# Performance work log

Hardware: AMD Instinct MI355X
Metric: run time of the kernel (lower is better)

The kernel has to match this reference:

```python
import jax, jax.numpy as jnp
from jax import lax
import numpy as np

# Module config (from init_kwargs / torch defaults)
CONF_THRES = 0.25
IOU_THRES = 0.45
MAX_DET = 300          # torch non_max_suppression max_det
BATCH = 16
N_PRED = 25200         # YOLOv5 anchors @ 640x640
NC = 80                # COCO classes
IMG = 640.0


def setup_inputs() -> dict:
    key = jax.random.key(0)
    k1, k2 = jax.random.split(key)
    # raw YOLO head output: [xywh (pixels), obj in [0,1], 80 class probs in [0,1]]
    prediction = jax.random.uniform(k1, (BATCH, N_PRED, NC + 5), dtype=jnp.float32)
    prediction = prediction.at[:, :, :4].multiply(IMG)  # realistic pixel-scale boxes
    logits = jax.random.normal(k2, (BATCH, N_PRED, NC), dtype=jnp.float32)
    return {"prediction": prediction, "logits": logits}


def _xywh2xyxy(x):
    xy, wh = x[..., :2], x[..., 2:4]
    return jnp.concatenate([xy - wh * 0.5, xy + wh * 0.5], axis=-1)


def _nms_image(pred, logit):
    """pred: [N, 85], logit: [N, 80] -> [MAX_DET, 87] padded detections.

    Row layout: [x1, y1, x2, y2, conf, cls, objectness, logits(80)].
    Invalid (padding) rows are zeroed, matching the variable-length torch output.
    """
    obj = pred[:, 4]                              # [N]
    cls_conf = pred[:, 5:] * obj[:, None]         # conf = cls_prob * obj  [N, 80]
    conf = jnp.max(cls_conf, axis=1)              # best-class confidence
    cls = jnp.argmax(cls_conf, axis=1)
    boxes = _xywh2xyxy(pred[:, :4])               # [N, 4] xyxy
    # candidate mask: obj > conf_thres (xc) AND best conf > conf_thres (conf_mask)
    valid = (obj > CONF_THRES) & (conf > CONF_THRES)
    scores0 = jnp.where(valid, conf, -jnp.inf)
    area = (boxes[:, 2] - boxes[:, 0]) * (boxes[:, 3] - boxes[:, 1])  # [N]

    # agnostic NMS (agnostic_nms=True -> no per-class box offset)
    def step(sc, _):
        idx = jnp.argmax(sc)                      # highest remaining score
        ok = jnp.isfinite(sc[idx])                # any candidate left?
        b = boxes[idx]
        lt = jnp.maximum(b[:2], boxes[:, :2])
        rb = jnp.minimum(b[2:], boxes[:, 2:])
        wh = jnp.clip(rb - lt, 0.0)
        inter = wh[:, 0] * wh[:, 1]
        iou = inter / (area[idx] + area - inter + 1e-9)
        sc = jnp.where(iou > IOU_THRES, -jnp.inf, sc)  # suppress (incl. self)
        return sc, (idx, ok)

    _, (sel, ok) = lax.scan(step, scores0, None, length=MAX_DET)

    det = jnp.concatenate(
        [boxes[sel], conf[sel][:, None], cls[sel][:, None].astype(jnp.float32),
         obj[sel][:, None], logit[sel]], axis=1)  # [MAX_DET, 87]
    return det * ok[:, None].astype(det.dtype)


def reference(prediction, logits):
    # [B, MAX_DET, 87]: xyxy(4) | conf | cls | objectness | class logits(80)
    return jax.vmap(_nms_image)(prediction, logits)
```

## Files before the change

kernel.cpp:

```cpp
#include <hip/hip_runtime.h>
#include <math.h>

#define NPRED  25200
#define BATCH  16
#define NC     80
#define MAXDET 300
#define NDIM   87
#define NBIN   1024

#define WS_SC      0
#define WS_BOX     1612800
#define WS_SELIDX  8064000
#define WS_SELCNT  8083200
#define WS_HIST    8083264
#define WS_CURSOR  8148800
#define WS_IA      8214336
#define WS_BINNED  8279872

#define PREP_TPB 256
#define PB 128

__global__ __launch_bounds__(PREP_TPB)
void prep_kernel(const float* __restrict__ pred,
                 float* __restrict__ sc,
                 float4* __restrict__ box,
                 unsigned int* __restrict__ hist) {
    __shared__ float4 s4[PB * 85 / 4];
    float* s = (float*)s4;
    const int t = threadIdx.x;
    const float4* p4 = (const float4*)(pred + (size_t)blockIdx.x * (PB * 85));
    for (int i = t; i < PB * 85 / 4; i += PREP_TPB) s4[i] = p4[i];
    __syncthreads();
    if (t < PB) {
        const float* row = s + t * 85;
        float x = row[0], y = row[1], w = row[2], h = row[3], obj = row[4];
        float best = -INFINITY;
        #pragma unroll 8
        for (int c = 0; c < NC; ++c) {
            float v = __fmul_rn(row[5 + c], obj);
            if (v > best) best = v;
        }
        float hw = __fmul_rn(w, 0.5f), hh = __fmul_rn(h, 0.5f);
        bool valid = (obj > 0.25f) && (best > 0.25f);
        int g = blockIdx.x * PB + t;
        sc[g]  = valid ? best : -INFINITY;
        box[g] = make_float4(__fsub_rn(x, hw), __fsub_rn(y, hh),
                             __fadd_rn(x, hw), __fadd_rn(y, hh));
        if (valid) {
            int img = g / NPRED;
            unsigned int sb = __float_as_uint(best);
            int bin = min((int)((sb - 0x3E800000u) >> 14), NBIN - 1);
            atomicAdd(&hist[img * NBIN + bin], 1u);
        }
    }
}

__global__ __launch_bounds__(NBIN)
void scan_kernel(const unsigned int* __restrict__ hist,
                 unsigned int* __restrict__ IaG,
                 unsigned int* __restrict__ cursor) {
    __shared__ unsigned int sA[NBIN], sB[NBIN];
    const int img = blockIdx.x, t = threadIdx.x;
    unsigned int cnt = hist[img * NBIN + t];
    sA[t] = cnt;
    __syncthreads();
    unsigned int *src = sA, *dst = sB;
    for (int d = 1; d < NBIN; d <<= 1) {
        dst[t] = src[t] + ((t + d) < NBIN ? src[t + d] : 0u);
        __syncthreads();
        unsigned int* tmp = src; src = dst; dst = tmp;
    }
    IaG[img * NBIN + t]    = src[t];
    cursor[img * NBIN + t] = src[t] - cnt;
}

#define SCB  16
#define STPB 512

__global__ __launch_bounds__(STPB)
void scatter_kernel(const float* __restrict__ sc,
                    unsigned int* __restrict__ cursor,
                    unsigned long long* __restrict__ binned) {
    const int img = blockIdx.x / SCB, part = blockIdx.x % SCB;
    const float* sci = sc + (size_t)img * NPRED;
    for (int e = part * STPB + threadIdx.x; e < NPRED; e += SCB * STPB) {
        float s = sci[e];
        if (s != -INFINITY) {
            unsigned int sb = __float_as_uint(s);
            int bin = min((int)((sb - 0x3E800000u) >> 14), NBIN - 1);
            unsigned int pos = atomicAdd(&cursor[img * NBIN + bin], 1u);
            binned[(size_t)img * NPRED + pos] =
                ((unsigned long long)(~sb) << 32) | (unsigned int)e;
        }
    }
}

#define TPB      1024
#define TCAP     4096
#define FIRSTCAP 1024
#define SLOTS    4
#define NW       (TPB / 64)

__device__ __forceinline__ bool iou_gt(float Bx1, float By1, float Bx2, float By2,
                                       float BA,
                                       float cx1, float cy1, float cx2, float cy2,
                                       float ca, double K) {
    float lx = fmaxf(Bx1, cx1), ly = fmaxf(By1, cy1);
    float rx = fminf(Bx2, cx2), ry = fminf(By2, cy2);
    float ww = fmaxf(__fsub_rn(rx, lx), 0.0f);
    float hh = fmaxf(__fsub_rn(ry, ly), 0.0f);
    float inter = __fmul_rn(ww, hh);
    float denom = __fadd_rn(__fsub_rn(__fadd_rn(BA, ca), inter), 1e-9f);
    return ((double)inter > K * (double)denom);
}

__device__ __forceinline__ int blk_min(int v, int* s_red, int t, int wid) {
    #pragma unroll
    for (int off = 32; off; off >>= 1) v = min(v, __shfl_down(v, off));
    if ((t & 63) == 0) s_red[wid] = v;
    __syncthreads();
    int r = s_red[0];
    #pragma unroll
    for (int w = 1; w < NW; ++w) r = min(r, s_red[w]);
    return r;
}

__global__ __launch_bounds__(TPB)
void nms_kernel(const unsigned long long* __restrict__ binned,
                const unsigned int* __restrict__ IaG,
                const float4* __restrict__ box_g,
                int* __restrict__ selidx,
                int* __restrict__ selcnt) {
    __shared__ unsigned long long sbuf[TCAP];
    __shared__ unsigned int IaL[NBIN];
    __shared__ float4 kbox[MAXDET];
    __shared__ float  karea[MAXDET];
    __shared__ unsigned char s_alive[TCAP];
    __shared__ int s_red[NW];
    __shared__ int s_kept, s_sticky, s_stickyIdx, s_fillFrom, s_cnt2;

    const int img = blockIdx.x, t = threadIdx.x, wid = t >> 6;
    const float4* bxi = box_g + (size_t)img * NPRED;
    const unsigned long long* bin_img = binned + (size_t)img * NPRED;
    const double K = (double)0.45f + 0x1p-26;

    IaL[t] = IaG[img * NBIN + t];
    if (t == 0) { s_kept = 0; s_sticky = 0; }
    __syncthreads();
    const int n_valid = (int)IaL[0];

    int o = 0, b_hi = NBIN;
    bool firstT = true;
    for (;;) {
        if (s_kept >= MAXDET || s_sticky || o >= n_valid) break;

        const int cap = firstT ? FIRSTCAP : TCAP;
        __syncthreads();
        int vb = (t < b_hi && ((int)IaL[t] - o) <= cap) ? t : 0x7FFFFFFF;
        int b_lo = blk_min(vb, s_red, t, wid);
        if (b_lo == 0x7FFFFFFF && cap != TCAP) {
            __syncthreads();
            vb = (t < b_hi && ((int)IaL[t] - o) <= TCAP) ? t : 0x7FFFFFFF;
            b_lo = blk_min(vb, s_red, t, wid);
        }
        int c;
        if (b_lo != 0x7FFFFFFF) {
            c = (int)IaL[b_lo] - o;
        } else {
            __syncthreads();
            vb = (t < b_hi && ((int)IaL[t] - o) > 0) ? -t : 0x7FFFFFFF;
            int m2 = blk_min(vb, s_red, t, wid);
            b_lo = -m2;
            c = min((int)IaL[b_lo] - o, TCAP);
        }
        if (c <= 0) break;

        unsigned int um = 0;
        unsigned long long ukey[SLOTS];
        #pragma unroll
        for (int s = 0; s < SLOTS; ++s) {
            int p = s * TPB + t;
            bool av = (p < c);
            ukey[s] = av ? bin_img[o + p] : ~0ULL;
            if (av) um |= (1u << s);
        }
        const int kept0 = s_kept;

        if (kept0 > 0 && um) {
            float ux1[SLOTS], uy1[SLOTS], ux2[SLOTS], uy2[SLOTS], uar[SLOTS];
            #pragma unroll
            for (int s = 0; s < SLOTS; ++s) {
                unsigned int ix = (um & (1u << s)) ? (unsigned int)ukey[s] : 0u;
                float4 b = bxi[ix];
                ux1[s] = b.x; uy1[s] = b.y; ux2[s] = b.z; uy2[s] = b.w;
                uar[s] = __fmul_rn(__fsub_rn(b.z, b.x), __fsub_rn(b.w, b.y));
            }
            for (int kb = 0; kb < kept0; ++kb) {
                float4 B = kbox[kb];
                float BA = karea[kb];
                #pragma unroll
                for (int s = 0; s < SLOTS; ++s) {
                    if (um & (1u << s)) {
                        if (iou_gt(B.x, B.y, B.z, B.w, BA,
                                   ux1[s], uy1[s], ux2[s], uy2[s], uar[s], K))
                            um &= ~(1u << s);
                    }
                }
                if (!um) break;
            }
        }
        if (t == 0) s_cnt2 = 0;
        __syncthreads();
        int cnt2;
        if (kept0 == 0) {
            #pragma unroll
            for (int s = 0; s < SLOTS; ++s) {
                int p = s * TPB + t;
                if (p < c) sbuf[p] = ukey[s];
            }
            cnt2 = c;
            __syncthreads();
        } else {
            #pragma unroll
            for (int s = 0; s < SLOTS; ++s)
                if (um & (1u << s)) sbuf[atomicAdd(&s_cnt2, 1)] = ukey[s];
            __syncthreads();
            cnt2 = s_cnt2;
        }

        if (cnt2 > 0) {
            int m = 1; while (m < cnt2) m <<= 1;
            for (int p = t; p < m; p += TPB) if (p >= cnt2) sbuf[p] = ~0ULL;
            __syncthreads();
            for (int k = 2; k <= m; k <<= 1) {
                for (int j = k >> 1; j > 0; j >>= 1) {
                    for (int i = t; i < m; i += TPB) {
                        int l = i ^ j;
                        if (l > i) {
                            unsigned long long a = sbuf[i], b2 = sbuf[l];
                            if ((a > b2) == ((i & k) == 0)) { sbuf[i] = b2; sbuf[l] = a; }
                        }
                    }
                    __syncthreads();
                }
            }
            unsigned int rm = 0;
            float rx1[SLOTS], ry1[SLOTS], rx2[SLOTS], ry2[SLOTS], rar[SLOTS];
            #pragma unroll
            for (int s = 0; s < SLOTS; ++s) {
                int p = t * SLOTS + s;
                bool av = (p < cnt2);
                unsigned int ix = av ? (unsigned int)sbuf[p] : 0u;
                float4 b = bxi[ix];
                rx1[s] = b.x; ry1[s] = b.y; rx2[s] = b.z; ry2[s] = b.w;
                rar[s] = __fmul_rn(__fsub_rn(b.z, b.x), __fsub_rn(b.w, b.y));
                if (av) rm |= (1u << s);
                s_alive[p] = av ? 1 : 0;
            }
            __syncthreads();

            const int nwin = (cnt2 + 63) >> 6;
            int applied = kept0;
            for (int g = 0; g < nwin; ++g) {
                int k0 = s_kept;
                if (rm) {
                    for (int kb = applied; kb < k0; ++kb) {
                        float4 B = kbox[kb];
                        float BA = karea[kb];
                        #pragma unroll
                        for (int s = 0; s < SLOTS; ++s) {
                            if (rm & (1u << s)) {
                                if (iou_gt(B.x, B.y, B.z, B.w, BA,
                                           rx1[s], ry1[s], rx2[s], ry2[s], rar[s], K)) {
                                    rm &= ~(1u << s);
                                    s_alive[t * SLOTS + s] = 0;
                                }
                            }
                        }
                        if (!rm) break;
                    }
                }
                applied = k0;
                __syncthreads();
                if (t < 64) {
                    int p = g * 64 + t;
                    int a = s_alive[p];
                    unsigned int ix = a ? (unsigned int)sbuf[p] : 0u;
                    float4 b = bxi[ix];
                    float cx1 = b.x, cy1 = b.y, cx2 = b.z, cy2 = b.w;
                    float car = __fmul_rn(__fsub_rn(b.z, b.x), __fsub_rn(b.w, b.y));
                    int kept = k0;
                    for (;;) {
                        unsigned long long bal = __ballot(a != 0);
                        if (!bal) break;
                        int f = (int)__builtin_ctzll(bal);
                        float Bx1 = __shfl(cx1, f), By1 = __shfl(cy1, f);
                        float Bx2 = __shfl(cx2, f), By2 = __shfl(cy2, f);
                        float BA  = __shfl(car, f);
                        int bidx  = __shfl((int)ix, f);
                        if (t == f) a = 0;
                        if (t == 0) {
                            selidx[img * MAXDET + kept] = bidx;
                            kbox[kept] = make_float4(Bx1, By1, Bx2, By2);
                            karea[kept] = BA;
                        }
                        float dns = __fadd_rn(__fsub_rn(__fadd_rn(BA, BA), BA), 1e-9f);
                        if (!((double)BA > K * (double)dns)) {
                            if (t == 0) { s_sticky = 1; s_stickyIdx = bidx; s_fillFrom = kept + 1; }
                            kept = MAXDET;
                            break;
                        }
                        if (a) {
                            if (iou_gt(Bx1, By1, Bx2, By2, BA,
                                       cx1, cy1, cx2, cy2, car, K)) a = 0;
                        }
                        ++kept;
                        if (kept >= MAXDET) break;
                    }
                    if (t == 0) s_kept = kept;
                }
                __syncthreads();
                if (((t * SLOTS) >> 6) == g) rm = 0;
                if (s_kept >= MAXDET || s_sticky) break;
            }
        }
        o = (int)IaL[b_lo];
        b_hi = b_lo;
        firstT = false;
    }
    int keptF = s_kept;
    if (s_sticky) {
        for (int k2 = s_fillFrom + t; k2 < MAXDET; k2 += TPB)
            selidx[img * MAXDET + k2] = s_stickyIdx;
        keptF = MAXDET;
    }
    if (t == 0) selcnt[img] = keptF;
}

#define GT 256

__global__ __launch_bounds__(GT)
void gather_kernel(const float* __restrict__ pred,
                   const float4* __restrict__ box,
                   const float* __restrict__ logits,
                   const int* __restrict__ selidx,
                   const int* __restrict__ selcnt,
                   float* __restrict__ out) {
    int tid = blockIdx.x * GT + threadIdx.x;
    if (tid >= BATCH * MAXDET * NDIM) return;
    int row = tid / NDIM, col = tid - row * NDIM;
    int img = row / MAXDET, det = row - img * MAXDET;
    float v = 0.0f;
    if (det < selcnt[img]) {
        int s = selidx[img * MAXDET + det];
        size_t g = (size_t)img * NPRED + s;
        if (col < 4) {
            float4 b = box[g];
            v = (col == 0) ? b.x : (col == 1) ? b.y : (col == 2) ? b.z : b.w;
        } else if (col == 6) {
            v = pred[g * 85 + 4];
        } else if (col >= 7) {
            v = logits[g * NC + (col - 7)];
        } else {
            const float* p = pred + g * 85;
            float obj = p[4];
            float best = -INFINITY; int bc = 0;
            #pragma unroll 8
            for (int c = 0; c < NC; ++c) {
                float q = __fmul_rn(p[5 + c], obj);
                if (q > best) { best = q; bc = c; }
            }
            v = (col == 4) ? best : (float)bc;
        }
    }
    out[tid] = v;
}

extern "C" void kernel_launch(void* const* d_in, const int* in_sizes, int n_in,
                              void* d_out, int out_size, void* d_ws, size_t ws_size,
                              hipStream_t stream) {
    const float* pred   = (const float*)d_in[0];
    const float* logits = (const float*)d_in[1];
    float* out = (float*)d_out;

    char* ws = (char*)d_ws;
    float*              sc     = (float*)(ws + WS_SC);
    float4*             box    = (float4*)(ws + WS_BOX);
    int*                selidx = (int*)(ws + WS_SELIDX);
    int*                selcnt = (int*)(ws + WS_SELCNT);
    unsigned int*       hist   = (unsigned int*)(ws + WS_HIST);
    unsigned int*       cursor = (unsigned int*)(ws + WS_CURSOR);
    unsigned int*       IaG    = (unsigned int*)(ws + WS_IA);
    unsigned long long* binned = (unsigned long long*)(ws + WS_BINNED);

    hipMemsetAsync(hist, 0, BATCH * NBIN * sizeof(unsigned int), stream);

    prep_kernel<<<BATCH * NPRED / PB, PREP_TPB, 0, stream>>>(pred, sc, box, hist);
    scan_kernel<<<BATCH, NBIN, 0, stream>>>(hist, IaG, cursor);
    scatter_kernel<<<BATCH * SCB, STPB, 0, stream>>>(sc, cursor, binned);
    nms_kernel<<<BATCH, TPB, 0, stream>>>(binned, IaG, box, selidx, selcnt);
    int gtot = BATCH * MAXDET * NDIM;
    gather_kernel<<<(gtot + GT - 1) / GT, GT, 0, stream>>>(pred, box, logits, selidx, selcnt, out);
}
```

Before: 303.8 us.

## Pre-sort histogram bins in a parallel kernel and drop in-loop bitonic sort

Adds a binsort kernel that sorts each score bin in place across many blocks, so the single-block-per-image NMS loop no longer runs a shared-memory bitonic sort on every tile. The NMS kernel now uses a contiguous per-wave slot layout with up to 8 slots per thread, ballot-based stream compaction instead of atomics, and greedy selection run inside a window wave that holds its boxes in registers. It also raises the tile capacity to 8192. The cost is one extra kernel launch over 16K blocks, more register pressure from 8 slots of box data, and partial-bin tile handling.

New measurement: 655.9 us. 2.16x slower.

```diff
diff --git a/kernel.cpp b/kernel.cpp
--- a/kernel.cpp
+++ b/kernel.cpp
@@ -95,10 +95,61 @@
     }
 }
 
+#define BS_TPB 256
+#define BS_CAP 4096
+
+__global__ __launch_bounds__(BS_TPB)
+void binsort_kernel(const unsigned int* __restrict__ hist,
+                    const unsigned int* __restrict__ IaG,
+                    unsigned long long* __restrict__ binned) {
+    __shared__ unsigned long long lds[BS_CAP];
+    const int img = blockIdx.x >> 10, b = blockIdx.x & (NBIN - 1);
+    const int t = threadIdx.x;
+    const int cnt = (int)hist[img * NBIN + b];
+    if (cnt <= 1) return;
+    const int start = (int)IaG[img * NBIN + b] - cnt;
+    unsigned long long* ptr = binned + (size_t)img * NPRED + start;
+
+    if (cnt <= 64) {
+        if (t < 64) {
+            unsigned long long key = (t < cnt) ? ptr[t] : ~0ULL;
+            #pragma unroll
+            for (int k = 2; k <= 64; k <<= 1) {
+                #pragma unroll
+                for (int j = k >> 1; j > 0; j >>= 1) {
+                    unsigned long long other = __shfl_xor(key, j);
+                    bool up = ((t & k) == 0), lower = ((t & j) == 0);
+                    unsigned long long mn = min(key, other), mx = max(key, other);
+                    key = (up == lower) ? mn : mx;
+                }
+            }
+            if (t < cnt) ptr[t] = key;
+        }
+        return;
+    }
+    const int cap = min(cnt, BS_CAP);
+    int m = 64; while (m < cap) m <<= 1;
+    for (int i = t; i < m; i += BS_TPB) lds[i] = (i < cap) ? ptr[i] : ~0ULL;
+    __syncthreads();
+    for (int k = 2; k <= m; k <<= 1) {
+        for (int j = k >> 1; j > 0; j >>= 1) {
+            for (int i = t; i < m; i += BS_TPB) {
+                int l = i ^ j;
+                if (l > i) {
+                    unsigned long long a = lds[i], b2 = lds[l];
+                    if ((a > b2) == ((i & k) == 0)) { lds[i] = b2; lds[l] = a; }
+                }
+            }
+            __syncthreads();
+        }
+    }
+    for (int i = t; i < cap; i += BS_TPB) ptr[i] = lds[i];
+}
+
 #define TPB      1024
-#define TCAP     4096
+#define TCAP     8192
 #define FIRSTCAP 1024
-#define SLOTS    4
+#define MAXS     8
 #define NW       (TPB / 64)
 
 __device__ __forceinline__ bool iou_gt(float Bx1, float By1, float Bx2, float By2,
@@ -115,6 +166,7 @@
 }
 
 __device__ __forceinline__ int blk_min(int v, int* s_red, int t, int wid) {
+    __syncthreads();
     #pragma unroll
     for (int off = 32; off; off >>= 1) v = min(v, __shfl_down(v, off));
     if ((t & 63) == 0) s_red[wid] = v;
@@ -135,14 +187,17 @@
     __shared__ unsigned int IaL[NBIN];
     __shared__ float4 kbox[MAXDET];
     __shared__ float  karea[MAXDET];
-    __shared__ unsigned char s_alive[TCAP];
     __shared__ int s_red[NW];
-    __shared__ int s_kept, s_sticky, s_stickyIdx, s_fillFrom, s_cnt2;
-
-    const int img = blockIdx.x, t = threadIdx.x, wid = t >> 6;
+    __shared__ unsigned int s_wsum[NW];
+    __shared__ int s_kept, s_sticky, s_stickyIdx, s_fillFrom;
+
+    const int img = blockIdx.x, t = threadIdx.x, wid = t >> 6, lane = t & 63;
     const float4* bxi = box_g + (size_t)img * NPRED;
     const unsigned long long* bin_img = binned + (size_t)img * NPRED;
     const double K = (double)0.45f + 0x1p-26;
+    const unsigned long long lmask = (lane == 63) ? ~0ULL >> 1 : (1ULL << (lane + 1)) - 1;
+    const unsigned long long below = lmask >> 1 << 1 >> 1;
+    (void)below;
 
     IaL[t] = IaG[img * NBIN + t];
     if (t == 0) { s_kept = 0; s_sticky = 0; }
@@ -152,14 +207,13 @@
     int o = 0, b_hi = NBIN;
     bool firstT = true;
     for (;;) {
+        __syncthreads();
         if (s_kept >= MAXDET || s_sticky || o >= n_valid) break;
 
         const int cap = firstT ? FIRSTCAP : TCAP;
-        __syncthreads();
         int vb = (t < b_hi && ((int)IaL[t] - o) <= cap) ? t : 0x7FFFFFFF;
         int b_lo = blk_min(vb, s_red, t, wid);
         if (b_lo == 0x7FFFFFFF && cap != TCAP) {
-            __syncthreads();
             vb = (t < b_hi && ((int)IaL[t] - o) <= TCAP) ? t : 0x7FFFFFFF;
             b_lo = blk_min(vb, s_red, t, wid);
         }
@@ -167,7 +221,6 @@
         if (b_lo != 0x7FFFFFFF) {
             c = (int)IaL[b_lo] - o;
         } else {
-            __syncthreads();
             vb = (t < b_hi && ((int)IaL[t] - o) > 0) ? -t : 0x7FFFFFFF;
             int m2 = blk_min(vb, s_red, t, wid);
             b_lo = -m2;
@@ -175,31 +228,30 @@
         }
         if (c <= 0) break;
 
+        const int S = (c + 1023) >> 10;
         unsigned int um = 0;
-        unsigned long long ukey[SLOTS];
+        unsigned long long ukey[MAXS];
+        float ux1[MAXS], uy1[MAXS], ux2[MAXS], uy2[MAXS], uar[MAXS];
         #pragma unroll
-        for (int s = 0; s < SLOTS; ++s) {
-            int p = s * TPB + t;
-            bool av = (p < c);
-            ukey[s] = av ? bin_img[o + p] : ~0ULL;
+        for (int s = 0; s < MAXS; ++s) {
+            int p = wid * (S << 6) + (s << 6) + lane;
+            bool av = (s < S) && (p < c);
+            unsigned long long key = av ? bin_img[o + p] : ~0ULL;
+            ukey[s] = key;
+            unsigned int ix = av ? (unsigned int)key : 0u;
+            float4 b = bxi[ix];
+            ux1[s] = b.x; uy1[s] = b.y; ux2[s] = b.z; uy2[s] = b.w;
+            uar[s] = __fmul_rn(__fsub_rn(b.z, b.x), __fsub_rn(b.w, b.y));
             if (av) um |= (1u << s);
         }
         const int kept0 = s_kept;
 
         if (kept0 > 0 && um) {
-            float ux1[SLOTS], uy1[SLOTS], ux2[SLOTS], uy2[SLOTS], uar[SLOTS];
-            #pragma unroll
-            for (int s = 0; s < SLOTS; ++s) {
-                unsigned int ix = (um & (1u << s)) ? (unsigned int)ukey[s] : 0u;
-                float4 b = bxi[ix];
-                ux1[s] = b.x; uy1[s] = b.y; ux2[s] = b.z; uy2[s] = b.w;
-                uar[s] = __fmul_rn(__fsub_rn(b.z, b.x), __fsub_rn(b.w, b.y));
-            }
             for (int kb = 0; kb < kept0; ++kb) {
                 float4 B = kbox[kb];
                 float BA = karea[kb];
                 #pragma unroll
-                for (int s = 0; s < SLOTS; ++s) {
+                for (int s = 0; s < MAXS; ++s) {
                     if (um & (1u << s)) {
                         if (iou_gt(B.x, B.y, B.z, B.w, BA,
                                    ux1[s], uy1[s], ux2[s], uy2[s], uar[s], K))
@@ -209,123 +261,124 @@
                 if (!um) break;
             }
         }
-        if (t == 0) s_cnt2 = 0;
+
+        int myoff[MAXS];
+        unsigned int wcnt = 0;
+        #pragma unroll
+        for (int s = 0; s < MAXS; ++s) {
+            unsigned long long bal = __ballot((int)((um >> s) & 1u));
+            unsigned long long lt = (lane == 0) ? 0ULL : (~0ULL >> (64 - lane));
+            myoff[s] = (int)(wcnt + __popcll(bal & lt));
+            wcnt += (unsigned int)__popcll(bal);
+        }
+        if (lane == 0) s_wsum[wid] = wcnt;
         __syncthreads();
-        int cnt2;
-        if (kept0 == 0) {
+        int wbase = 0, cnt2 = 0;
+        #pragma unroll
+        for (int w = 0; w < NW; ++w) {
+            int v = (int)s_wsum[w];
+            if (w < wid) wbase += v;
+            cnt2 += v;
+        }
+        #pragma unroll
+        for (int s = 0; s < MAXS; ++s)
+            if (um & (1u << s)) sbuf[wbase + myoff[s]] = ukey[s];
+        __syncthreads();
+
+        if (cnt2 > 0) {
+            const int S2 = (cnt2 >= 512) ? 8 : max(1, (cnt2 + 63) >> 6);
+            const int W = S2 << 6;
+            const int nwin = (cnt2 + W - 1) / W;
+            unsigned int rm = 0;
+            unsigned int rIdx[MAXS];
+            float rx1[MAXS], ry1[MAXS], rx2[MAXS], ry2[MAXS], rar[MAXS];
             #pragma unroll
-            for (int s = 0; s < SLOTS; ++s) {
-                int p = s * TPB + t;
-                if (p < c) sbuf[p] = ukey[s];
-            }
-            cnt2 = c;
-            __syncthreads();
-        } else {
-            #pragma unroll
-            for (int s = 0; s < SLOTS; ++s)
-                if (um & (1u << s)) sbuf[atomicAdd(&s_cnt2, 1)] = ukey[s];
-            __syncthreads();
-            cnt2 = s_cnt2;
-        }
-
-        if (cnt2 > 0) {
-            int m = 1; while (m < cnt2) m <<= 1;
-            for (int p = t; p < m; p += TPB) if (p >= cnt2) sbuf[p] = ~0ULL;
-            __syncthreads();
-            for (int k = 2; k <= m; k <<= 1) {
-                for (int j = k >> 1; j > 0; j >>= 1) {
-                    for (int i = t; i < m; i += TPB) {
-                        int l = i ^ j;
-                        if (l > i) {
-                            unsigned long long a = sbuf[i], b2 = sbuf[l];
-                            if ((a > b2) == ((i & k) == 0)) { sbuf[i] = b2; sbuf[l] = a; }
-                        }
-                    }
-                    __syncthreads();
-                }
-            }
-            unsigned int rm = 0;
-            float rx1[SLOTS], ry1[SLOTS], rx2[SLOTS], ry2[SLOTS], rar[SLOTS];
-            #pragma unroll
-            for (int s = 0; s < SLOTS; ++s) {
-                int p = t * SLOTS + s;
-                bool av = (p < cnt2);
-                unsigned int ix = av ? (unsigned int)sbuf[p] : 0u;
+            for (int s = 0; s < MAXS; ++s) {
+                int p = wid * W + (s << 6) + lane;
+                bool av = (s < S2) && (p < cnt2);
+                unsigned long long key = av ? sbuf[p] : ~0ULL;
+                unsigned int ix = av ? (unsigned int)key : 0u;
+                rIdx[s] = ix;
                 float4 b = bxi[ix];
                 rx1[s] = b.x; ry1[s] = b.y; rx2[s] = b.z; ry2[s] = b.w;
                 rar[s] = __fmul_rn(__fsub_rn(b.z, b.x), __fsub_rn(b.w, b.y));
                 if (av) rm |= (1u << s);
-                s_alive[p] = av ? 1 : 0;
-            }
-            __syncthreads();
-
-            const int nwin = (cnt2 + 63) >> 6;
-            int applied = kept0;
+            }
+
             for (int g = 0; g < nwin; ++g) {
-                int k0 = s_kept;
+                const int k0 = s_kept;
+                if (wid == g) {
+                    int kept = k0;
+                    for (;;) {
+                        int bestp = 0x7FFFFFFF;
+                        #pragma unroll
+                        for (int s = 0; s < MAXS; ++s) {
+                            if (s < S2) {
+                                unsigned long long bal = __ballot((int)((rm >> s) & 1u));
+                                if (bal) bestp = min(bestp, (s << 6) | (int)__builtin_ctzll(bal));
+                            }
+                        }
+                        if (bestp == 0x7FFFFFFF) break;
+                        const int fs = bestp >> 6, f = bestp & 63;
+                        float Bx1 = 0, By1 = 0, Bx2 = 0, By2 = 0, BA = 0; int bidx = 0;
+                        #pragma unroll
+                        for (int s = 0; s < MAXS; ++s) if (s == fs) {
+                            Bx1 = __shfl(rx1[s], f); By1 = __shfl(ry1[s], f);
+                            Bx2 = __shfl(rx2[s], f); By2 = __shfl(ry2[s], f);
+                            BA  = __shfl(rar[s], f); bidx = __shfl((int)rIdx[s], f);
+                        }
+                        if (lane == f) rm &= ~(1u << fs);
+                        if (lane == 0) {
+                            selidx[img * MAXDET + kept] = bidx;
+                            kbox[kept] = make_float4(Bx1, By1, Bx2, By2);
+                            karea[kept] = BA;
+                        }
+                        float dns = __fadd_rn(__fsub_rn(__fadd_rn(BA, BA), BA), 1e-9f);
+                        if (!((double)BA > K * (double)dns)) {
+                            if (lane == 0) { s_sticky = 1; s_stickyIdx = bidx; s_fillFrom = kept + 1; }
+                            kept = MAXDET;
+                            break;
+                        }
+                        #pragma unroll
+                        for (int s = 0; s < MAXS; ++s) {
+                            if (s < S2) {
+                                if (__ballot((int)((rm >> s) & 1u))) {
+                                    if ((rm >> s) & 1u) {
+                                        if (iou_gt(Bx1, By1, Bx2, By2, BA,
+                                                   rx1[s], ry1[s], rx2[s], ry2[s], rar[s], K))
+                                            rm &= ~(1u << s);
+                                    }
+                                }
+                            }
+                        }
+                        ++kept;
+                        if (kept >= MAXDET) break;
+                    }
+                    if (lane == 0) s_kept = kept;
+                }
+                __syncthreads();
+                if (s_sticky || s_kept >= MAXDET) break;
+                const int k1 = s_kept;
                 if (rm) {
-                    for (int kb = applied; kb < k0; ++kb) {
+                    for (int kb = k0; kb < k1; ++kb) {
                         float4 B = kbox[kb];
                         float BA = karea[kb];
                         #pragma unroll
-                        for (int s = 0; s < SLOTS; ++s) {
+                        for (int s = 0; s < MAXS; ++s) {
                             if (rm & (1u << s)) {
                                 if (iou_gt(B.x, B.y, B.z, B.w, BA,
-                                           rx1[s], ry1[s], rx2[s], ry2[s], rar[s], K)) {
+                                           rx1[s], ry1[s], rx2[s], ry2[s], rar[s], K))
                                     rm &= ~(1u << s);
-                                    s_alive[t * SLOTS + s] = 0;
-                                }
                             }
                         }
                         if (!rm) break;
                     }
                 }
-                applied = k0;
                 __syncthreads();
-                if (t < 64) {
-                    int p = g * 64 + t;
-                    int a = s_alive[p];
-                    unsigned int ix = a ? (unsigned int)sbuf[p] : 0u;
-                    float4 b = bxi[ix];
-                    float cx1 = b.x, cy1 = b.y, cx2 = b.z, cy2 = b.w;
-                    float car = __fmul_rn(__fsub_rn(b.z, b.x), __fsub_rn(b.w, b.y));
-                    int kept = k0;
-                    for (;;) {
-                        unsigned long long bal = __ballot(a != 0);
-                        if (!bal) break;
-                        int f = (int)__builtin_ctzll(bal);
-                        float Bx1 = __shfl(cx1, f), By1 = __shfl(cy1, f);
-                        float Bx2 = __shfl(cx2, f), By2 = __shfl(cy2, f);
-                        float BA  = __shfl(car, f);
-                        int bidx  = __shfl((int)ix, f);
-                        if (t == f) a = 0;
-                        if (t == 0) {
-                            selidx[img * MAXDET + kept] = bidx;
-                            kbox[kept] = make_float4(Bx1, By1, Bx2, By2);
-                            karea[kept] = BA;
-                        }
-                        float dns = __fadd_rn(__fsub_rn(__fadd_rn(BA, BA), BA), 1e-9f);
-                        if (!((double)BA > K * (double)dns)) {
-                            if (t == 0) { s_sticky = 1; s_stickyIdx = bidx; s_fillFrom = kept + 1; }
-                            kept = MAXDET;
-                            break;
-                        }
-                        if (a) {
-                            if (iou_gt(Bx1, By1, Bx2, By2, BA,
-                                       cx1, cy1, cx2, cy2, car, K)) a = 0;
-                        }
-                        ++kept;
-                        if (kept >= MAXDET) break;
-                    }
-                    if (t == 0) s_kept = kept;
-                }
-                __syncthreads();
-                if (((t * SLOTS) >> 6) == g) rm = 0;
-                if (s_kept >= MAXDET || s_sticky) break;
-            }
-        }
-        o = (int)IaL[b_lo];
-        b_hi = b_lo;
+            }
+        }
+        o += c;
+        if (o >= (int)IaL[b_lo]) b_hi = b_lo;
         firstT = false;
     }
     int keptF = s_kept;
@@ -398,6 +451,7 @@
     prep_kernel<<<BATCH * NPRED / PB, PREP_TPB, 0, stream>>>(pred, sc, box, hist);
     scan_kernel<<<BATCH, NBIN, 0, stream>>>(hist, IaG, cursor);
     scatter_kernel<<<BATCH * SCB, STPB, 0, stream>>>(sc, cursor, binned);
+    binsort_kernel<<<BATCH * NBIN, BS_TPB, 0, stream>>>(hist, IaG, binned);
     nms_kernel<<<BATCH, TPB, 0, stream>>>(binned, IaG, box, selidx, selcnt);
     int gtot = BATCH * MAXDET * NDIM;
     gather_kernel<<<(gtot + GT - 1) / GT, GT, 0, stream>>>(pred, box, logits, selidx, selcnt, out);
```

## Pre-sort score bins in parallel kernel and drop in-block bitonic sort from NMS

Applied to the files above, without the earlier changes.

Adds a binsort kernel that sorts each histogram bin of candidates in parallel across many blocks, using wave shuffles for small bins and LDS bitonic sort for larger ones. The NMS kernel can then skip its serial per-tile bitonic sort, since the keys already arrive in order. The atomic compaction of survivors is replaced by an order-preserving ballot/popcount prefix compaction, and the tile loads are reorganised per wave. The cost is an extra launch of 16K blocks, most of which exit immediately. Bins larger than 4096 entries are only partially sorted, which may be a correctness risk for degenerate inputs.

Measured after the change: 321.6 us. 5.8% more time.

```diff
diff --git a/kernel.cpp b/kernel.cpp
--- a/kernel.cpp
+++ b/kernel.cpp
@@ -95,6 +95,57 @@
     }
 }
 
+#define BS_TPB 256
+#define BS_CAP 4096
+
+__global__ __launch_bounds__(BS_TPB)
+void binsort_kernel(const unsigned int* __restrict__ hist,
+                    const unsigned int* __restrict__ IaG,
+                    unsigned long long* __restrict__ binned) {
+    __shared__ unsigned long long lds[BS_CAP];
+    const int img = blockIdx.x >> 10, b = blockIdx.x & (NBIN - 1);
+    const int t = threadIdx.x;
+    const int cnt = (int)hist[img * NBIN + b];
+    if (cnt <= 1) return;
+    const int start = (int)IaG[img * NBIN + b] - cnt;
+    unsigned long long* ptr = binned + (size_t)img * NPRED + start;
+
+    if (cnt <= 64) {
+        if (t < 64) {
+            unsigned long long key = (t < cnt) ? ptr[t] : ~0ULL;
+            #pragma unroll
+            for (int k = 2; k <= 64; k <<= 1) {
+                #pragma unroll
+                for (int j = k >> 1; j > 0; j >>= 1) {
+                    unsigned long long other = __shfl_xor(key, j);
+                    bool up = ((t & k) == 0), lower = ((t & j) == 0);
+                    unsigned long long mn = min(key, other), mx = max(key, other);
+                    key = (up == lower) ? mn : mx;
+                }
+            }
+            if (t < cnt) ptr[t] = key;
+        }
+        return;
+    }
+    const int cap = min(cnt, BS_CAP);
+    int m = 64; while (m < cap) m <<= 1;
+    for (int i = t; i < m; i += BS_TPB) lds[i] = (i < cap) ? ptr[i] : ~0ULL;
+    __syncthreads();
+    for (int k = 2; k <= m; k <<= 1) {
+        for (int j = k >> 1; j > 0; j >>= 1) {
+            for (int i = t; i < m; i += BS_TPB) {
+                int l = i ^ j;
+                if (l > i) {
+                    unsigned long long a = lds[i], b2 = lds[l];
+                    if ((a > b2) == ((i & k) == 0)) { lds[i] = b2; lds[l] = a; }
+                }
+            }
+            __syncthreads();
+        }
+    }
+    for (int i = t; i < cap; i += BS_TPB) ptr[i] = lds[i];
+}
+
 #define TPB      1024
 #define TCAP     4096
 #define FIRSTCAP 1024
@@ -115,6 +166,7 @@
 }
 
 __device__ __forceinline__ int blk_min(int v, int* s_red, int t, int wid) {
+    __syncthreads();
     #pragma unroll
     for (int off = 32; off; off >>= 1) v = min(v, __shfl_down(v, off));
     if ((t & 63) == 0) s_red[wid] = v;
@@ -137,9 +189,10 @@
     __shared__ float  karea[MAXDET];
     __shared__ unsigned char s_alive[TCAP];
     __shared__ int s_red[NW];
-    __shared__ int s_kept, s_sticky, s_stickyIdx, s_fillFrom, s_cnt2;
-
-    const int img = blockIdx.x, t = threadIdx.x, wid = t >> 6;
+    __shared__ unsigned int s_wsum[NW];
+    __shared__ int s_kept, s_sticky, s_stickyIdx, s_fillFrom;
+
+    const int img = blockIdx.x, t = threadIdx.x, wid = t >> 6, lane = t & 63;
     const float4* bxi = box_g + (size_t)img * NPRED;
     const unsigned long long* bin_img = binned + (size_t)img * NPRED;
     const double K = (double)0.45f + 0x1p-26;
@@ -152,14 +205,13 @@
     int o = 0, b_hi = NBIN;
     bool firstT = true;
     for (;;) {
+        __syncthreads();
         if (s_kept >= MAXDET || s_sticky || o >= n_valid) break;
 
         const int cap = firstT ? FIRSTCAP : TCAP;
-        __syncthreads();
         int vb = (t < b_hi && ((int)IaL[t] - o) <= cap) ? t : 0x7FFFFFFF;
         int b_lo = blk_min(vb, s_red, t, wid);
         if (b_lo == 0x7FFFFFFF && cap != TCAP) {
-            __syncthreads();
             vb = (t < b_hi && ((int)IaL[t] - o) <= TCAP) ? t : 0x7FFFFFFF;
             b_lo = blk_min(vb, s_red, t, wid);
         }
@@ -167,7 +219,6 @@
         if (b_lo != 0x7FFFFFFF) {
             c = (int)IaL[b_lo] - o;
         } else {
-            __syncthreads();
             vb = (t < b_hi && ((int)IaL[t] - o) > 0) ? -t : 0x7FFFFFFF;
             int m2 = blk_min(vb, s_red, t, wid);
             b_lo = -m2;
@@ -175,75 +226,65 @@
         }
         if (c <= 0) break;
 
+        const int kept0 = s_kept;
+
+        const int S = (c + 1023) >> 10;
         unsigned int um = 0;
         unsigned long long ukey[SLOTS];
-        #pragma unroll
-        for (int s = 0; s < SLOTS; ++s) {
-            int p = s * TPB + t;
-            bool av = (p < c);
-            ukey[s] = av ? bin_img[o + p] : ~0ULL;
-            if (av) um |= (1u << s);
-        }
-        const int kept0 = s_kept;
-
-        if (kept0 > 0 && um) {
+        {
             float ux1[SLOTS], uy1[SLOTS], ux2[SLOTS], uy2[SLOTS], uar[SLOTS];
             #pragma unroll
             for (int s = 0; s < SLOTS; ++s) {
-                unsigned int ix = (um & (1u << s)) ? (unsigned int)ukey[s] : 0u;
+                int p = wid * (S << 6) + (s << 6) + lane;
+                bool av = (s < S) && (p < c);
+                unsigned long long key = av ? bin_img[o + p] : ~0ULL;
+                ukey[s] = key;
+                unsigned int ix = av ? (unsigned int)key : 0u;
                 float4 b = bxi[ix];
                 ux1[s] = b.x; uy1[s] = b.y; ux2[s] = b.z; uy2[s] = b.w;
                 uar[s] = __fmul_rn(__fsub_rn(b.z, b.x), __fsub_rn(b.w, b.y));
-            }
-            for (int kb = 0; kb < kept0; ++kb) {
-                float4 B = kbox[kb];
-                float BA = karea[kb];
-                #pragma unroll
-                for (int s = 0; s < SLOTS; ++s) {
-                    if (um & (1u << s)) {
-                        if (iou_gt(B.x, B.y, B.z, B.w, BA,
-                                   ux1[s], uy1[s], ux2[s], uy2[s], uar[s], K))
-                            um &= ~(1u << s);
-                    }
-                }
-                if (!um) break;
-            }
-        }
-        if (t == 0) s_cnt2 = 0;
-        __syncthreads();
-        int cnt2;
-        if (kept0 == 0) {
-            #pragma unroll
-            for (int s = 0; s < SLOTS; ++s) {
-                int p = s * TPB + t;
-                if (p < c) sbuf[p] = ukey[s];
-            }
-            cnt2 = c;
-            __syncthreads();
-        } else {
-            #pragma unroll
-            for (int s = 0; s < SLOTS; ++s)
-                if (um & (1u << s)) sbuf[atomicAdd(&s_cnt2, 1)] = ukey[s];
-            __syncthreads();
-            cnt2 = s_cnt2;
-        }
-
-        if (cnt2 > 0) {
-            int m = 1; while (m < cnt2) m <<= 1;
-            for (int p = t; p < m; p += TPB) if (p >= cnt2) sbuf[p] = ~0ULL;
-            __syncthreads();
-            for (int k = 2; k <= m; k <<= 1) {
-                for (int j = k >> 1; j > 0; j >>= 1) {
-                    for (int i = t; i < m; i += TPB) {
-                        int l = i ^ j;
-                        if (l > i) {
-                            unsigned long long a = sbuf[i], b2 = sbuf[l];
-                            if ((a > b2) == ((i & k) == 0)) { sbuf[i] = b2; sbuf[l] = a; }
+                if (av) um |= (1u << s);
+            }
+            if (kept0 > 0 && um) {
+                for (int kb = 0; kb < kept0; ++kb) {
+                    float4 B = kbox[kb];
+                    float BA = karea[kb];
+                    #pragma unroll
+                    for (int s = 0; s < SLOTS; ++s) {
+                        if (um & (1u << s)) {
+                            if (iou_gt(B.x, B.y, B.z, B.w, BA,
+                                       ux1[s], uy1[s], ux2[s], uy2[s], uar[s], K))
+                                um &= ~(1u << s);
                         }
                     }
-                    __syncthreads();
+                    if (!um) break;
                 }
             }
+        }
+        int myoff[SLOTS];
+        unsigned int wcnt = 0;
+        const unsigned long long lt = (lane == 0) ? 0ULL : (~0ULL >> (64 - lane));
+        #pragma unroll
+        for (int s = 0; s < SLOTS; ++s) {
+            unsigned long long bal = __ballot((int)((um >> s) & 1u));
+            myoff[s] = (int)(wcnt + __popcll(bal & lt));
+            wcnt += (unsigned int)__popcll(bal);
+        }
+        if (lane == 0) s_wsum[wid] = wcnt;
+        __syncthreads();
+        int wbase = 0, cnt2 = 0;
+        #pragma unroll
+        for (int w = 0; w < NW; ++w) {
+            int v = (int)s_wsum[w];
+            if (w < wid) wbase += v;
+            cnt2 += v;
+        }
+        #pragma unroll
+        for (int s = 0; s < SLOTS; ++s)
+            if (um & (1u << s)) sbuf[wbase + myoff[s]] = ukey[s];
+        __syncthreads();
+
+        if (cnt2 > 0) {
             unsigned int rm = 0;
             float rx1[SLOTS], ry1[SLOTS], rx2[SLOTS], ry2[SLOTS], rar[SLOTS];
             #pragma unroll
@@ -324,8 +365,8 @@
                 if (s_kept >= MAXDET || s_sticky) break;
             }
         }
-        o = (int)IaL[b_lo];
-        b_hi = b_lo;
+        o += c;
+        if (o >= (int)IaL[b_lo]) b_hi = b_lo;
         firstT = false;
     }
     int keptF = s_kept;
@@ -398,6 +439,7 @@
     prep_kernel<<<BATCH * NPRED / PB, PREP_TPB, 0, stream>>>(pred, sc, box, hist);
     scan_kernel<<<BATCH, NBIN, 0, stream>>>(hist, IaG, cursor);
     scatter_kernel<<<BATCH * SCB, STPB, 0, stream>>>(sc, cursor, binned);
+    binsort_kernel<<<BATCH * NBIN, BS_TPB, 0, stream>>>(hist, IaG, binned);
     nms_kernel<<<BATCH, TPB, 0, stream>>>(binned, IaG, box, selidx, selcnt);
     int gtot = BATCH * MAXDET * NDIM;
     gather_kernel<<<(gtot + GT - 1) / GT, GT, 0, stream>>>(pred, box, logits, selidx, selcnt, out);
```
